# Optimization experiments

Hardware: AMD Instinct MI355X
Metric: run time of the kernel (lower is better)

Reference implementation:

```python
import jax, jax.numpy as jnp
import numpy as np

D_MODEL = 512
N_HEADS = 8
D_FF = 2048
EPS = 1e-6


def layer_norm(x, g, b):
    mu = jnp.mean(x, axis=-1, keepdims=True)
    var = jnp.mean(jnp.square(x - mu), axis=-1, keepdims=True)
    return (x - mu) * jax.lax.rsqrt(var + EPS) * g + b


def setup_inputs() -> dict:
    key = jax.random.key(0)
    ks = jax.random.split(key, 6)
    B, S = 64, 500
    x = jax.random.normal(ks[0], (B, S, D_MODEL), dtype=jnp.float32)
    ln1_g = jnp.ones((D_MODEL,), jnp.float32)
    ln1_b = jnp.zeros((D_MODEL,), jnp.float32)
    ln2_g = jnp.ones((D_MODEL,), jnp.float32)
    ln2_b = jnp.zeros((D_MODEL,), jnp.float32)
    W1 = jax.random.normal(ks[1], (D_MODEL, D_FF), jnp.float32) * (1.0 / np.sqrt(D_MODEL))
    b1 = jnp.zeros((D_FF,), jnp.float32)
    W2 = jax.random.normal(ks[2], (D_FF, D_MODEL), jnp.float32) * (1.0 / np.sqrt(D_FF))
    b2 = jnp.zeros((D_MODEL,), jnp.float32)
    return {"x": x, "ln1_g": ln1_g, "ln1_b": ln1_b, "ln2_g": ln2_g, "ln2_b": ln2_b,
            "W1": W1, "b1": b1, "W2": W2, "b2": b2}


def causal_attention(h):
    # h: [B, S, D]; q=k=v=h (no projections in this module)
    B, S, D = h.shape
    Hd = D // N_HEADS
    qkv = h.reshape(B, S, N_HEADS, Hd).transpose(0, 2, 1, 3)  # [B, H, S, Hd]
    w = jnp.einsum('bhsd,bhtd->bhst', qkv, qkv) / jnp.sqrt(jnp.float32(Hd))
    mask = jnp.tril(jnp.ones((S, S), dtype=bool))
    w = jnp.where(mask, w, jnp.finfo(w.dtype).min)
    w = jax.nn.softmax(w, axis=-1)
    out = jnp.einsum('bhst,bhtd->bhsd', w, qkv)  # [B, H, S, Hd]
    return out.transpose(0, 2, 1, 3).reshape(B, S, D)


def reference(x, ln1_g, ln1_b, ln2_g, ln2_b, W1, b1, W2, b2):
    # Pre-LN block, but residuals attach to the post-LN activations (faithful to source).
    h = layer_norm(x, ln1_g, ln1_b)
    h = h + causal_attention(h)
    h2 = layer_norm(h, ln2_g, ln2_b)
    ff = jnp.maximum(h2 @ W1 + b1, 0.0) @ W2 + b2
    return h2 + ff
```

## Files before the change

kernel.cpp:

```cpp
#include <hip/hip_runtime.h>
#include <hip/hip_bf16.h>

#define D_MODEL 512
#define N_HEADS 8
#define HDIM 64
#define D_FF 2048
#define BATCH 64
#define SEQ 500
#define MROWS (BATCH * SEQ)

typedef __attribute__((ext_vector_type(8))) short bhalf8;
typedef __attribute__((ext_vector_type(4))) float floatx4;

#define AS_GLOBAL __attribute__((address_space(1)))
#define AS_LDS __attribute__((address_space(3)))

__device__ __forceinline__ void glds16(const void* g, void* l) {
  __builtin_amdgcn_global_load_lds((const AS_GLOBAL unsigned int*)g,
                                   (AS_LDS unsigned int*)l, 16, 0, 0);
}

__device__ __forceinline__ unsigned short f2bf(float f) {
  __hip_bfloat16 b = __float2bfloat16(f);
  return *reinterpret_cast<unsigned short*>(&b);
}

template <int MODE>
__global__ __launch_bounds__(256) void ln_kernel(const void* __restrict__ xin,
                                                 const float* __restrict__ g,
                                                 const float* __restrict__ b,
                                                 float* __restrict__ yf,
                                                 __hip_bfloat16* __restrict__ yb) {
  int row = blockIdx.x;
  int t = threadIdx.x;
  float v0, v1;
  if constexpr (MODE == 0) {
    float2 v = ((const float2*)xin)[(size_t)row * 256 + t];
    v0 = v.x; v1 = v.y;
  } else {
    __hip_bfloat162 bv = ((const __hip_bfloat162*)xin)[(size_t)row * 256 + t];
    v0 = __bfloat162float(bv.x); v1 = __bfloat162float(bv.y);
  }
  float s = v0 + v1;
  float sq = v0 * v0 + v1 * v1;
#pragma unroll
  for (int off = 32; off > 0; off >>= 1) {
    s += __shfl_down(s, off, 64);
    sq += __shfl_down(sq, off, 64);
  }
  __shared__ float red[8];
  if ((t & 63) == 0) {
    red[(t >> 6) * 2] = s;
    red[(t >> 6) * 2 + 1] = sq;
  }
  __syncthreads();
  s = red[0] + red[2] + red[4] + red[6];
  sq = red[1] + red[3] + red[5] + red[7];
  float mean = s * (1.0f / 512.0f);
  float var = sq * (1.0f / 512.0f) - mean * mean;
  float r = rsqrtf(var + 1e-6f);
  float2 gg = ((const float2*)g)[t];
  float2 bb = ((const float2*)b)[t];
  float y0 = (v0 - mean) * r * gg.x + bb.x;
  float y1 = (v1 - mean) * r * gg.y + bb.y;
  if constexpr (MODE == 1)
    ((float2*)yf)[(size_t)row * 256 + t] = make_float2(y0, y1);
  __hip_bfloat162 bv2;
  bv2.x = __float2bfloat16(y0);
  bv2.y = __float2bfloat16(y1);
  ((__hip_bfloat162*)yb)[(size_t)row * 256 + t] = bv2;
}

__global__ __launch_bounds__(256) void transpose_bf16(const float* __restrict__ W,
                                                      __hip_bfloat16* __restrict__ Wt,
                                                      int K, int N) {
  __shared__ float tile[32][33];
  int n0 = blockIdx.x * 32, k0 = blockIdx.y * 32;
  int tx = threadIdx.x, ty = threadIdx.y;
#pragma unroll
  for (int j = 0; j < 32; j += 8)
    tile[ty + j][tx] = W[(size_t)(k0 + ty + j) * N + n0 + tx];
  __syncthreads();
#pragma unroll
  for (int j = 0; j < 32; j += 8)
    Wt[(size_t)(n0 + ty + j) * K + k0 + tx] = __float2bfloat16(tile[tx][ty + j]);
}

__device__ __forceinline__ void attn_tile_step(int jq, int kt, int fr, int kg,
                                               const char* Kb, const char* Vb,
                                               char* Pw, bhalf8 (&qf)[2][2],
                                               floatx4 (&O)[2][4], float (&l)[2][4]) {
  int roff = 32 * jq - 64 * kt;
  bool domask = (jq <= 2 * kt + 1);
#pragma unroll
  for (int mr = 0; mr < 2; ++mr) {
    floatx4 S[4];
#pragma unroll
    for (int nc = 0; nc < 4; ++nc) S[nc] = (floatx4){0.f, 0.f, 0.f, 0.f};
    __builtin_amdgcn_s_setprio(1);
#pragma unroll
    for (int kk = 0; kk < 2; ++kk) {
#pragma unroll
      for (int nc = 0; nc < 4; ++nc) {
        bhalf8 kf = *(const bhalf8*)(Kb + (nc * 16 + fr) * 128 +
                                     (((kk * 4 + kg) ^ (fr & 7)) << 4));
        S[nc] = __builtin_amdgcn_mfma_f32_16x16x32_bf16(qf[mr][kk], kf, S[nc], 0, 0, 0);
      }
    }
    __builtin_amdgcn_s_setprio(0);
    if (domask) {
#pragma unroll
      for (int nc = 0; nc < 4; ++nc)
#pragma unroll
        for (int j = 0; j < 4; ++j)
          if (nc * 16 + fr > roff + mr * 16 + kg * 4 + j) S[nc][j] = -INFINITY;
    }
    float p[4][4], rs[4];
#pragma unroll
    for (int j = 0; j < 4; ++j) rs[j] = 0.f;
#pragma unroll
    for (int nc = 0; nc < 4; ++nc)
#pragma unroll
      for (int j = 0; j < 4; ++j) {
        p[nc][j] = __expf(S[nc][j] * 0.125f - 66.0f);
        rs[j] += p[nc][j];
      }
#pragma unroll
    for (int off = 1; off < 16; off <<= 1)
#pragma unroll
      for (int j = 0; j < 4; ++j) rs[j] += __shfl_xor(rs[j], off, 64);
#pragma unroll
    for (int j = 0; j < 4; ++j) l[mr][j] += rs[j];
#pragma unroll
    for (int nc = 0; nc < 4; ++nc)
#pragma unroll
      for (int j = 0; j < 4; ++j)
        *(unsigned short*)(Pw + ((kg * 4 + j) * 72 + nc * 16 + fr) * 2) = f2bf(p[nc][j]);
    __builtin_amdgcn_s_setprio(1);
#pragma unroll
    for (int kk = 0; kk < 2; ++kk) {
      bhalf8 pf = *(const bhalf8*)(Pw + fr * 144 + kk * 64 + kg * 16);
#pragma unroll
      for (int nc = 0; nc < 4; ++nc) {
        bhalf8 vf = *(const bhalf8*)(Vb + (nc * 16 + fr) * 144 + kk * 64 + kg * 16);
        O[mr][nc] = __builtin_amdgcn_mfma_f32_16x16x32_bf16(pf, vf, O[mr][nc], 0, 0, 0);
      }
    }
    __builtin_amdgcn_s_setprio(0);
  }
}

__global__ __launch_bounds__(512) void attn_fold(const __hip_bfloat16* __restrict__ hbp,
                                                 __hip_bfloat16* __restrict__ hres) {
  __shared__ unsigned short Ks[2][64 * 64];
  __shared__ unsigned short Vt[2][64 * 72];
  __shared__ unsigned short Ps[8][16 * 72];

  int blk = blockIdx.x;
  int b = blk >> 3, hd = blk & 7;
  int tid = threadIdx.x;
  int w = tid >> 6, lane = tid & 63;
  int fr = lane & 15, kg = lane >> 4;

  const unsigned short* hb = (const unsigned short*)hbp;
  size_t bbase = (size_t)b * SEQ * D_MODEL + hd * HDIM;

  int jH = 15 - w, jL = w;
  bhalf8 qH[2][2], qL[2][2];
#pragma unroll
  for (int mr = 0; mr < 2; ++mr) {
    int rH = 32 * jH + mr * 16 + fr;
    if (rH >= SEQ) rH = SEQ - 1;
    int rL = 32 * jL + mr * 16 + fr;
#pragma unroll
    for (int kk = 0; kk < 2; ++kk) {
      qH[mr][kk] = *(const bhalf8*)(hb + bbase + (size_t)rH * D_MODEL + kk * 32 + kg * 8);
      qL[mr][kk] = *(const bhalf8*)(hb + bbase + (size_t)rL * D_MODEL + kk * 32 + kg * 8);
    }
  }

  floatx4 OH[2][4], OL[2][4];
  float lHs[2][4], lLs[2][4];
#pragma unroll
  for (int mr = 0; mr < 2; ++mr)
#pragma unroll
    for (int nc = 0; nc < 4; ++nc) {
      OH[mr][nc] = (floatx4){0.f, 0.f, 0.f, 0.f};
      OL[mr][nc] = (floatx4){0.f, 0.f, 0.f, 0.f};
    }
#pragma unroll
  for (int mr = 0; mr < 2; ++mr)
#pragma unroll
    for (int j = 0; j < 4; ++j) { lHs[mr][j] = 0.f; lLs[mr][j] = 0.f; }

  int krow = w * 8 + (lane >> 3);
  int scb = (lane & 7) ^ (lane >> 3);

  {
    glds16(hb + bbase + (size_t)krow * D_MODEL + scb * 8, (char*)Ks[0] + w * 1024);
    bhalf8 v0 = *(const bhalf8*)(hb + bbase + (size_t)lane * D_MODEL + w * 8);
#pragma unroll
    for (int i = 0; i < 8; ++i) Vt[0][(w * 8 + i) * 72 + lane] = (unsigned short)v0[i];
  }
  __syncthreads();

  for (int kt = 0; kt < 8; ++kt) {
    int cur = kt & 1;
    bhalf8 vnext;
    if (kt < 7) {
      int sr = (kt + 1) * 64 + krow;
      if (sr >= SEQ) sr = SEQ - 1;
      glds16(hb + bbase + (size_t)sr * D_MODEL + scb * 8, (char*)Ks[cur ^ 1] + w * 1024);
      int vr = (kt + 1) * 64 + lane;
      if (vr >= SEQ) vr = SEQ - 1;
      vnext = *(const bhalf8*)(hb + bbase + (size_t)vr * D_MODEL + w * 8);
    }

    const char* Kb = (const char*)Ks[cur];
    const char* Vb = (const char*)Vt[cur];
    char* Pw = (char*)Ps[w];
    if (jH >= 2 * kt) attn_tile_step(jH, kt, fr, kg, Kb, Vb, Pw, qH, OH, lHs);
    if (jL >= 2 * kt) attn_tile_step(jL, kt, fr, kg, Kb, Vb, Pw, qL, OL, lLs);

    if (kt < 7) {
#pragma unroll
      for (int i = 0; i < 8; ++i)
        Vt[cur ^ 1][(w * 8 + i) * 72 + lane] = (unsigned short)vnext[i];
    }
    __syncthreads();
  }

#pragma unroll
  for (int mr = 0; mr < 2; ++mr)
#pragma unroll
    for (int j = 0; j < 4; ++j) {
      int qH_row = 32 * jH + mr * 16 + kg * 4 + j;
      if (qH_row < SEQ) {
        float inv = 1.0f / lHs[mr][j];
        size_t ro = bbase + (size_t)qH_row * D_MODEL;
#pragma unroll
        for (int nc = 0; nc < 4; ++nc) {
          size_t idx = ro + nc * 16 + fr;
          float hv = __bfloat162float(hbp[idx]);
          hres[idx] = __float2bfloat16(hv + OH[mr][nc][j] * inv);
        }
      }
      int qL_row = 32 * jL + mr * 16 + kg * 4 + j;
      {
        float inv = 1.0f / lLs[mr][j];
        size_t ro = bbase + (size_t)qL_row * D_MODEL;
#pragma unroll
        for (int nc = 0; nc < 4; ++nc) {
          size_t idx = ro + nc * 16 + fr;
          float hv = __bfloat162float(hbp[idx]);
          hres[idx] = __float2bfloat16(hv + OL[mr][nc][j] * inv);
        }
      }
    }
}

template <int EPI>
__global__ __launch_bounds__(512) void gemmbk64(const unsigned short* __restrict__ A,
                                                const unsigned short* __restrict__ Bt,
                                                const float* __restrict__ bias,
                                                float* __restrict__ outf,
                                                __hip_bfloat16* __restrict__ outb,
                                                int M, int N, int K, int gx) {
  __shared__ __align__(16) char smem[2 * 65536];

  int nwg = gridDim.x;
  int bid = blockIdx.x;
  int q = nwg >> 3, r = nwg & 7;
  int xcd = bid & 7, lo = bid >> 3;
  int wg = (xcd < r ? xcd * (q + 1) : r * (q + 1) + (xcd - r) * q) + lo;
  int by = wg / gx, bx = wg % gx;
  int m0 = by * 256, n0 = bx * 256;

  int tid = threadIdx.x;
  int w = tid >> 6, lane = tid & 63;
  int wm = w >> 2, wn = w & 3;
  int fr = lane & 15, kg = lane >> 4;

  int srow = lane >> 3;
  int scol = ((lane & 7) ^ srow) * 8;
  const unsigned short* Ag0 = A + (size_t)(m0 + (w)*8 + srow) * K + scol;
  const unsigned short* Ag1 = A + (size_t)(m0 + (w + 8) * 8 + srow) * K + scol;
  const unsigned short* Ag2 = A + (size_t)(m0 + (w + 16) * 8 + srow) * K + scol;
  const unsigned short* Ag3 = A + (size_t)(m0 + (w + 24) * 8 + srow) * K + scol;
  const unsigned short* Bg0 = Bt + (size_t)(n0 + (w)*8 + srow) * K + scol;
  const unsigned short* Bg1 = Bt + (size_t)(n0 + (w + 8) * 8 + srow) * K + scol;
  const unsigned short* Bg2 = Bt + (size_t)(n0 + (w + 16) * 8 + srow) * K + scol;
  const unsigned short* Bg3 = Bt + (size_t)(n0 + (w + 24) * 8 + srow) * K + scol;

  int slot0 = ((kg ^ (fr & 7)) << 4);
  int slot1 = (((4 + kg) ^ (fr & 7)) << 4);
  int abase = (wm * 128 + fr) * 128;
  int bbase = 32768 + (wn * 64 + fr) * 128;

  floatx4 acc[8][4];
#pragma unroll
  for (int i = 0; i < 8; ++i)
#pragma unroll
    for (int j = 0; j < 4; ++j) acc[i][j] = (floatx4){0.f, 0.f, 0.f, 0.f};

  int nt = K >> 6;

#define STAGE(t, buf)                                       \
  {                                                         \
    char* d = smem + (buf)*65536;                           \
    glds16(Ag0 + (size_t)(t)*64, d + (w)*1024);             \
    glds16(Ag1 + (size_t)(t)*64, d + (w + 8) * 1024);       \
    glds16(Ag2 + (size_t)(t)*64, d + (w + 16) * 1024);      \
    glds16(Ag3 + (size_t)(t)*64, d + (w + 24) * 1024);      \
    glds16(Bg0 + (size_t)(t)*64, d + 32768 + (w)*1024);     \
    glds16(Bg1 + (size_t)(t)*64, d + 32768 + (w + 8) * 1024); \
    glds16(Bg2 + (size_t)(t)*64, d + 32768 + (w + 16) * 1024); \
    glds16(Bg3 + (size_t)(t)*64, d + 32768 + (w + 24) * 1024); \
  }

  STAGE(0, 0);
  asm volatile("s_waitcnt vmcnt(0)" ::: "memory");
  __builtin_amdgcn_s_barrier();

  for (int t = 0; t < nt; ++t) {
    const char* bufp = smem + (t & 1) * 65536;
    if (t + 1 < nt) STAGE(t + 1, (t + 1) & 1);
    __builtin_amdgcn_sched_barrier(0);

    bhalf8 bfr[2][4];
#pragma unroll
    for (int nn = 0; nn < 4; ++nn) {
      bfr[0][nn] = *(const bhalf8*)(bufp + bbase + nn * 2048 + slot0);
      bfr[1][nn] = *(const bhalf8*)(bufp + bbase + nn * 2048 + slot1);
    }
    __builtin_amdgcn_s_setprio(1);
#pragma unroll
    for (int mm = 0; mm < 8; ++mm) {
      bhalf8 a0 = *(const bhalf8*)(bufp + abase + mm * 2048 + slot0);
#pragma unroll
      for (int nn = 0; nn < 4; ++nn)
        acc[mm][nn] =
            __builtin_amdgcn_mfma_f32_16x16x32_bf16(a0, bfr[0][nn], acc[mm][nn], 0, 0, 0);
      bhalf8 a1 = *(const bhalf8*)(bufp + abase + mm * 2048 + slot1);
#pragma unroll
      for (int nn = 0; nn < 4; ++nn)
        acc[mm][nn] =
            __builtin_amdgcn_mfma_f32_16x16x32_bf16(a1, bfr[1][nn], acc[mm][nn], 0, 0, 0);
    }
    __builtin_amdgcn_s_setprio(0);
    if (t + 1 < nt) asm volatile("s_waitcnt vmcnt(0)" ::: "memory");
    __builtin_amdgcn_s_barrier();
  }
#undef STAGE

  int grow_base = m0 + wm * 128 + kg * 4;
  int gcol_base = n0 + wn * 64 + fr;
#pragma unroll
  for (int mm = 0; mm < 8; ++mm) {
#pragma unroll
    for (int nn = 0; nn < 4; ++nn) {
      int gc = gcol_base + nn * 16;
      float bi = bias[gc];
#pragma unroll
      for (int j = 0; j < 4; ++j) {
        int gr = grow_base + mm * 16 + j;
        float v = acc[mm][nn][j] + bi;
        if (EPI == 1) {
          v = v > 0.f ? v : 0.f;
          outb[(size_t)gr * N + gc] = __float2bfloat16(v);
        } else {
          size_t idx = (size_t)gr * N + gc;
          outf[idx] = outf[idx] + v;
        }
      }
    }
  }
}

extern "C" void kernel_launch(void* const* d_in, const int* in_sizes, int n_in,
                              void* d_out, int out_size, void* d_ws, size_t ws_size,
                              hipStream_t stream) {
  const float* x = (const float*)d_in[0];
  const float* ln1g = (const float*)d_in[1];
  const float* ln1b = (const float*)d_in[2];
  const float* ln2g = (const float*)d_in[3];
  const float* ln2b = (const float*)d_in[4];
  const float* W1 = (const float*)d_in[5];
  const float* b1 = (const float*)d_in[6];
  const float* W2 = (const float*)d_in[7];
  const float* b2 = (const float*)d_in[8];
  float* out = (float*)d_out;

  char* ws = (char*)d_ws;
  __hip_bfloat16* h2b = (__hip_bfloat16*)ws;
  __hip_bfloat16* hb = (__hip_bfloat16*)(ws + 65536000);
  __hip_bfloat16* hresb = (__hip_bfloat16*)(ws + 98304000);
  __hip_bfloat16* u = (__hip_bfloat16*)(ws + 98304000);
  __hip_bfloat16* W1t = (__hip_bfloat16*)(ws + 229376000);
  __hip_bfloat16* W2t = (__hip_bfloat16*)(ws + 231473152);

  transpose_bf16<<<dim3(D_FF / 32, D_MODEL / 32), dim3(32, 8), 0, stream>>>(
      W1, W1t, D_MODEL, D_FF);
  transpose_bf16<<<dim3(D_MODEL / 32, D_FF / 32), dim3(32, 8), 0, stream>>>(
      W2, W2t, D_FF, D_MODEL);

  ln_kernel<0><<<MROWS, 256, 0, stream>>>(x, ln1g, ln1b, nullptr, hb);

  attn_fold<<<BATCH * N_HEADS, 512, 0, stream>>>(hb, hresb);

  ln_kernel<1><<<MROWS, 256, 0, stream>>>(hresb, ln2g, ln2b, out, h2b);

  gemmbk64<1><<<(MROWS / 256) * (D_FF / 256), 512, 0, stream>>>(
      (const unsigned short*)h2b, (const unsigned short*)W1t, b1, nullptr, u,
      MROWS, D_FF, D_MODEL, D_FF / 256);
  gemmbk64<2><<<(MROWS / 256) * (D_MODEL / 256), 512, 0, stream>>>(
      (const unsigned short*)u, (const unsigned short*)W2t, b2, out, nullptr,
      MROWS, D_MODEL, D_FF, D_MODEL / 256);
}
```

Measured before the change: 322.2 us.

## Replace 256x256 double-buffered GEMM with smaller single-buffered 128x128 multi-occupancy GEMM

Swaps the FFN GEMM kernel from a 256x256 tile, 512-thread, double-buffered K=64 design to a 128x128 tile, 256-thread kernel with K=32 steps, a single 16KB LDS buffer, and launch bounds allowing three blocks per CU. Latency hiding now comes from running several blocks per CU instead of software pipelining, and the finer tiles give more blocks for load balance. In exchange each tile reuses its operands less, and each K step waits on its loads behind two barriers with no prefetch.

```diff
diff --git a/kernel.cpp b/kernel.cpp
--- a/kernel.cpp
+++ b/kernel.cpp
@@ -260,13 +260,13 @@
 }
 
 template <int EPI>
-__global__ __launch_bounds__(512) void gemmbk64(const unsigned short* __restrict__ A,
-                                                const unsigned short* __restrict__ Bt,
-                                                const float* __restrict__ bias,
-                                                float* __restrict__ outf,
-                                                __hip_bfloat16* __restrict__ outb,
-                                                int M, int N, int K, int gx) {
-  __shared__ __align__(16) char smem[2 * 65536];
+__global__ __launch_bounds__(256, 3) void gemm97(const unsigned short* __restrict__ A,
+                                                 const unsigned short* __restrict__ Bt,
+                                                 const float* __restrict__ bias,
+                                                 float* __restrict__ outf,
+                                                 __hip_bfloat16* __restrict__ outb,
+                                                 int M, int N, int K, int gx) {
+  __shared__ __align__(16) char smem[16384];
 
   int nwg = gridDim.x;
   int bid = blockIdx.x;
@@ -274,89 +274,60 @@
   int xcd = bid & 7, lo = bid >> 3;
   int wg = (xcd < r ? xcd * (q + 1) : r * (q + 1) + (xcd - r) * q) + lo;
   int by = wg / gx, bx = wg % gx;
-  int m0 = by * 256, n0 = bx * 256;
+  int m0 = by * 128, n0 = bx * 128;
 
   int tid = threadIdx.x;
   int w = tid >> 6, lane = tid & 63;
-  int wm = w >> 2, wn = w & 3;
+  int wr = (w >> 1) * 64, wc = (w & 1) * 64;
   int fr = lane & 15, kg = lane >> 4;
 
-  int srow = lane >> 3;
-  int scol = ((lane & 7) ^ srow) * 8;
-  const unsigned short* Ag0 = A + (size_t)(m0 + (w)*8 + srow) * K + scol;
-  const unsigned short* Ag1 = A + (size_t)(m0 + (w + 8) * 8 + srow) * K + scol;
-  const unsigned short* Ag2 = A + (size_t)(m0 + (w + 16) * 8 + srow) * K + scol;
-  const unsigned short* Ag3 = A + (size_t)(m0 + (w + 24) * 8 + srow) * K + scol;
-  const unsigned short* Bg0 = Bt + (size_t)(n0 + (w)*8 + srow) * K + scol;
-  const unsigned short* Bg1 = Bt + (size_t)(n0 + (w + 8) * 8 + srow) * K + scol;
-  const unsigned short* Bg2 = Bt + (size_t)(n0 + (w + 16) * 8 + srow) * K + scol;
-  const unsigned short* Bg3 = Bt + (size_t)(n0 + (w + 24) * 8 + srow) * K + scol;
-
-  int slot0 = ((kg ^ (fr & 7)) << 4);
-  int slot1 = (((4 + kg) ^ (fr & 7)) << 4);
-  int abase = (wm * 128 + fr) * 128;
-  int bbase = 32768 + (wn * 64 + fr) * 128;
-
-  floatx4 acc[8][4];
-#pragma unroll
-  for (int i = 0; i < 8; ++i)
+  int srow = lane >> 2;
+  int scol = ((lane & 3) ^ ((lane >> 3) & 3)) * 8;
+  const unsigned short* Ag0 = A + (size_t)(m0 + w * 16 + srow) * K + scol;
+  const unsigned short* Ag1 = A + (size_t)(m0 + (w + 4) * 16 + srow) * K + scol;
+  const unsigned short* Bg0 = Bt + (size_t)(n0 + w * 16 + srow) * K + scol;
+  const unsigned short* Bg1 = Bt + (size_t)(n0 + (w + 4) * 16 + srow) * K + scol;
+  char* dA0 = smem + w * 1024;
+  char* dA1 = smem + (w + 4) * 1024;
+  char* dB0 = smem + 8192 + w * 1024;
+  char* dB1 = smem + 8192 + (w + 4) * 1024;
+
+  int swz16 = (kg ^ ((fr >> 1) & 3)) << 4;
+  const char* abase = smem + (wr + fr) * 64 + swz16;
+  const char* bbase = smem + 8192 + (wc + fr) * 64 + swz16;
+
+  floatx4 acc[4][4];
+#pragma unroll
+  for (int i = 0; i < 4; ++i)
 #pragma unroll
     for (int j = 0; j < 4; ++j) acc[i][j] = (floatx4){0.f, 0.f, 0.f, 0.f};
 
-  int nt = K >> 6;
-
-#define STAGE(t, buf)                                       \
-  {                                                         \
-    char* d = smem + (buf)*65536;                           \
-    glds16(Ag0 + (size_t)(t)*64, d + (w)*1024);             \
-    glds16(Ag1 + (size_t)(t)*64, d + (w + 8) * 1024);       \
-    glds16(Ag2 + (size_t)(t)*64, d + (w + 16) * 1024);      \
-    glds16(Ag3 + (size_t)(t)*64, d + (w + 24) * 1024);      \
-    glds16(Bg0 + (size_t)(t)*64, d + 32768 + (w)*1024);     \
-    glds16(Bg1 + (size_t)(t)*64, d + 32768 + (w + 8) * 1024); \
-    glds16(Bg2 + (size_t)(t)*64, d + 32768 + (w + 16) * 1024); \
-    glds16(Bg3 + (size_t)(t)*64, d + 32768 + (w + 24) * 1024); \
-  }
-
-  STAGE(0, 0);
-  asm volatile("s_waitcnt vmcnt(0)" ::: "memory");
-  __builtin_amdgcn_s_barrier();
-
+  int nt = K >> 5;
   for (int t = 0; t < nt; ++t) {
-    const char* bufp = smem + (t & 1) * 65536;
-    if (t + 1 < nt) STAGE(t + 1, (t + 1) & 1);
-    __builtin_amdgcn_sched_barrier(0);
-
-    bhalf8 bfr[2][4];
-#pragma unroll
-    for (int nn = 0; nn < 4; ++nn) {
-      bfr[0][nn] = *(const bhalf8*)(bufp + bbase + nn * 2048 + slot0);
-      bfr[1][nn] = *(const bhalf8*)(bufp + bbase + nn * 2048 + slot1);
-    }
-    __builtin_amdgcn_s_setprio(1);
-#pragma unroll
-    for (int mm = 0; mm < 8; ++mm) {
-      bhalf8 a0 = *(const bhalf8*)(bufp + abase + mm * 2048 + slot0);
+    glds16(Ag0 + (size_t)t * 32, dA0);
+    glds16(Ag1 + (size_t)t * 32, dA1);
+    glds16(Bg0 + (size_t)t * 32, dB0);
+    glds16(Bg1 + (size_t)t * 32, dB1);
+    __syncthreads();
+
+    bhalf8 av[4], bv[4];
+#pragma unroll
+    for (int mm = 0; mm < 4; ++mm) av[mm] = *(const bhalf8*)(abase + mm * 1024);
+#pragma unroll
+    for (int nn = 0; nn < 4; ++nn) bv[nn] = *(const bhalf8*)(bbase + nn * 1024);
+#pragma unroll
+    for (int mm = 0; mm < 4; ++mm)
 #pragma unroll
       for (int nn = 0; nn < 4; ++nn)
         acc[mm][nn] =
-            __builtin_amdgcn_mfma_f32_16x16x32_bf16(a0, bfr[0][nn], acc[mm][nn], 0, 0, 0);
-      bhalf8 a1 = *(const bhalf8*)(bufp + abase + mm * 2048 + slot1);
-#pragma unroll
-      for (int nn = 0; nn < 4; ++nn)
-        acc[mm][nn] =
-            __builtin_amdgcn_mfma_f32_16x16x32_bf16(a1, bfr[1][nn], acc[mm][nn], 0, 0, 0);
-    }
-    __builtin_amdgcn_s_setprio(0);
-    if (t + 1 < nt) asm volatile("s_waitcnt vmcnt(0)" ::: "memory");
-    __builtin_amdgcn_s_barrier();
-  }
-#undef STAGE
-
-  int grow_base = m0 + wm * 128 + kg * 4;
-  int gcol_base = n0 + wn * 64 + fr;
-#pragma unroll
-  for (int mm = 0; mm < 8; ++mm) {
+            __builtin_amdgcn_mfma_f32_16x16x32_bf16(av[mm], bv[nn], acc[mm][nn], 0, 0, 0);
+    __syncthreads();
+  }
+
+  int grow_base = m0 + wr + kg * 4;
+  int gcol_base = n0 + wc + fr;
+#pragma unroll
+  for (int mm = 0; mm < 4; ++mm) {
 #pragma unroll
     for (int nn = 0; nn < 4; ++nn) {
       int gc = gcol_base + nn * 16;
@@ -410,10 +381,10 @@
 
   ln_kernel<1><<<MROWS, 256, 0, stream>>>(hresb, ln2g, ln2b, out, h2b);
 
-  gemmbk64<1><<<(MROWS / 256) * (D_FF / 256), 512, 0, stream>>>(
+  gemm97<1><<<(MROWS / 128) * (D_FF / 128), 256, 0, stream>>>(
       (const unsigned short*)h2b, (const unsigned short*)W1t, b1, nullptr, u,
-      MROWS, D_FF, D_MODEL, D_FF / 256);
-  gemmbk64<2><<<(MROWS / 256) * (D_MODEL / 256), 512, 0, stream>>>(
+      MROWS, D_FF, D_MODEL, D_FF / 128);
+  gemm97<2><<<(MROWS / 128) * (D_MODEL / 128), 256, 0, stream>>>(
       (const unsigned short*)u, (const unsigned short*)W2t, b2, out, nullptr,
-      MROWS, D_MODEL, D_FF, D_MODEL / 256);
-}
+      MROWS, D_MODEL, D_FF, D_MODEL / 128);
+}
```

New measurement: 310.5 us. -3.6%, faster.
